# Optimization experiments

Measured on AMD Instinct MI355X. Metric: run time of the kernel, lower is better.

The kernel has to match this reference:

```python
import jax, jax.numpy as jnp
import numpy as np


def setup_inputs() -> dict:
    key = jax.random.key(0)
    k1, k2, k3, k4 = jax.random.split(key, 4)
    B, F, E = 8, 64, 50000
    Cout, K = 128, 5
    x = jax.random.normal(k1, (B, F, E), dtype=jnp.float32)
    gemm = jax.random.randint(k2, (B, E, 4), 0, E, dtype=jnp.int64)  # 1-ring neighbor edge indices
    fan_in = F * K
    W = jax.random.normal(k3, (Cout, F, 1, K), dtype=jnp.float32) / np.sqrt(fan_in)
    b = jax.random.normal(k4, (Cout,), dtype=jnp.float32) * 0.01
    return {"x": x, "gemm": gemm, "W": W, "b": b}


def reference(x, gemm, W, b):
    # x: [B, F, E] edge features; gemm: [B, E, 4] neighbor indices in [0, E)
    B, F, E = x.shape
    # pad_gemm prepends the edge's own index as column 0; create_gemm shifts by +1
    # and pads x with a zero column at index 0 (slot for missing / -1 neighbors).
    xp = jnp.concatenate([jnp.zeros((B, F, 1), dtype=x.dtype), x], axis=2)  # [B, F, E+1]
    self_idx = jnp.broadcast_to(jnp.arange(E, dtype=gemm.dtype)[None, :, None], (B, E, 1))
    idx = jnp.concatenate([self_idx, gemm], axis=2) + 1  # [B, E, 5], indices into E+1 slots
    # gather: f[b, f, e, k] = xp[b, f, idx[b, e, k]]
    xp_t = jnp.transpose(xp, (0, 2, 1))  # [B, E+1, F]
    f = jnp.take_along_axis(xp_t, idx.reshape(B, E * 5, 1), axis=1)  # [B, E*5, F]
    f = jnp.transpose(f.reshape(B, E, 5, F), (0, 3, 1, 2))  # [B, F, E, 5]
    # symmetric (order-invariant) pooling over the 4 neighbors
    x0 = f[:, :, :, 0]
    x1 = f[:, :, :, 1] + f[:, :, :, 3]
    x2 = f[:, :, :, 2] + f[:, :, :, 4]
    x3 = jnp.abs(f[:, :, :, 1] - f[:, :, :, 3])
    x4 = jnp.abs(f[:, :, :, 2] - f[:, :, :, 4])
    G = jnp.stack([x0, x1, x2, x3, x4], axis=3)  # [B, F, E, 5]
    # Conv2d with kernel (1, 5) over width-5 map == contraction over (F, 5)
    out = jnp.einsum('bfek,ofk->boe', G, W[:, :, 0, :]) + b[None, :, None]
    return out[..., None]  # [B, Cout, E, 1]
```

## Files before the change

kernel.cpp:

```cpp
#include <hip/hip_runtime.h>
#include <hip/hip_bf16.h>

#define NB 8
#define NF 64
#define NE 50000
#define NO 128
#define TE 64
#define NK 320
#define KSTEPS 10

typedef short short8 __attribute__((ext_vector_type(8)));
typedef float f32x4 __attribute__((ext_vector_type(4)));

__device__ __forceinline__ unsigned short f2bf(float x) {
    union { float f; unsigned int u; } v; v.f = x;
    unsigned int r = v.u + 0x7fffu + ((v.u >> 16) & 1u);
    return (unsigned short)(r >> 16);
}

__global__ __launch_bounds__(256) void transpose_x(
    const float* __restrict__ x, float* __restrict__ xT, int E)
{
    __shared__ float tile[64][65];
    int ntiles = (E + 63) >> 6;
    int b = blockIdx.x / ntiles;
    int t = blockIdx.x % ntiles;
    int e0 = t << 6;
    int le = threadIdx.x & 63;
    int q  = threadIdx.x >> 6;
    const float* xb = x + (size_t)b * NF * E;
    #pragma unroll
    for (int i = 0; i < 16; ++i) {
        int f = q * 16 + i;
        int e = e0 + le;
        tile[f][le] = (e < E) ? xb[(size_t)f * E + e] : 0.0f;
    }
    __syncthreads();
    float* xTb = xT + (size_t)b * E * NF;
    #pragma unroll
    for (int i = 0; i < 16; ++i) {
        int el = q * 16 + i;
        int e = e0 + el;
        if (e < E) xTb[(size_t)e * NF + le] = tile[le][el];
    }
}

__global__ __launch_bounds__(256) void prep_w(
    const float* __restrict__ W, unsigned short* __restrict__ Wt)
{
    int idx = blockIdx.x * 256 + threadIdx.x;
    if (idx >= NK * NO) return;
    int K = idx >> 7;
    int o = idx & 127;
    int f  = K & 63;
    int kp = K >> 6;
    float v = W[(size_t)o * (NF * 5) + f * 5 + kp];
    Wt[((size_t)(K >> 3) * NO + o) * 8 + (K & 7)] = f2bf(v);
}

__global__ __launch_bounds__(256) void conv_main(
    const float* __restrict__ xsrc,
    const int* __restrict__ gemm,
    const unsigned short* __restrict__ Wt,
    const float* __restrict__ bias,
    float* __restrict__ out,
    int E, int useXT)
{
    __shared__ __align__(16) unsigned short Gs[NK * TE];

    int ntiles = (E + TE - 1) / TE;
    int b     = blockIdx.x / ntiles;
    int etile = blockIdx.x % ntiles;
    int tid = threadIdx.x;

    {
        int ge = tid >> 2;
        int j  = tid & 3;
        int e  = etile * TE + ge;
        bool valid = (e < E);
        int gi[5];
        if (valid) {
            gi[0] = e;
            const int* gp = gemm + ((size_t)b * E + e) * 4;
            gi[1] = gp[0]; gi[2] = gp[1]; gi[3] = gp[2]; gi[4] = gp[3];
        }
        #pragma unroll
        for (int h = 0; h < 2; ++h) {
            int f0 = j * 16 + h * 8;
            float c[5][8];
            if (valid) {
                if (useXT) {
                    #pragma unroll
                    for (int k = 0; k < 5; ++k) {
                        const float* p = xsrc + ((size_t)b * E + gi[k]) * NF + f0;
                        float4 v0 = *(const float4*)p;
                        float4 v1 = *(const float4*)(p + 4);
                        c[k][0] = v0.x; c[k][1] = v0.y; c[k][2] = v0.z; c[k][3] = v0.w;
                        c[k][4] = v1.x; c[k][5] = v1.y; c[k][6] = v1.z; c[k][7] = v1.w;
                    }
                } else {
                    #pragma unroll
                    for (int k = 0; k < 5; ++k)
                        #pragma unroll
                        for (int i = 0; i < 8; ++i)
                            c[k][i] = xsrc[(size_t)b * NF * E + (size_t)(f0 + i) * E + gi[k]];
                }
            } else {
                #pragma unroll
                for (int k = 0; k < 5; ++k)
                    #pragma unroll
                    for (int i = 0; i < 8; ++i) c[k][i] = 0.0f;
            }
            float g[5][8];
            #pragma unroll
            for (int i = 0; i < 8; ++i) {
                g[0][i] = c[0][i];
                g[1][i] = c[1][i] + c[3][i];
                g[2][i] = c[2][i] + c[4][i];
                g[3][i] = fabsf(c[1][i] - c[3][i]);
                g[4][i] = fabsf(c[2][i] - c[4][i]);
            }
            #pragma unroll
            for (int kp = 0; kp < 5; ++kp) {
                int kblk = kp * 8 + j * 2 + h;
                uint4 pk;
                pk.x = (unsigned)f2bf(g[kp][0]) | ((unsigned)f2bf(g[kp][1]) << 16);
                pk.y = (unsigned)f2bf(g[kp][2]) | ((unsigned)f2bf(g[kp][3]) << 16);
                pk.z = (unsigned)f2bf(g[kp][4]) | ((unsigned)f2bf(g[kp][5]) << 16);
                pk.w = (unsigned)f2bf(g[kp][6]) | ((unsigned)f2bf(g[kp][7]) << 16);
                *(uint4*)&Gs[((size_t)kblk * TE + ge) * 8] = pk;
            }
        }
    }
    __syncthreads();

    int wave = tid >> 6;
    int lane = tid & 63;
    int l16 = lane & 15;
    int lq  = lane >> 4;
    int mh = (wave >> 1) * 4;
    int np = (wave & 1) * 2;

    f32x4 acc[4][2];
    #pragma unroll
    for (int mt = 0; mt < 4; ++mt)
        #pragma unroll
        for (int nt = 0; nt < 2; ++nt)
            acc[mt][nt] = (f32x4){0.f, 0.f, 0.f, 0.f};

    for (int ks = 0; ks < KSTEPS; ++ks) {
        short8 a[4], bb[2];
        #pragma unroll
        for (int mt = 0; mt < 4; ++mt) {
            int o = (mh + mt) * 16 + l16;
            a[mt] = *(const short8*)&Wt[((size_t)(ks * 4 + lq) * NO + o) * 8];
        }
        #pragma unroll
        for (int nt = 0; nt < 2; ++nt) {
            int el = (np + nt) * 16 + l16;
            bb[nt] = *(const short8*)&Gs[((size_t)(ks * 4 + lq) * TE + el) * 8];
        }
        #pragma unroll
        for (int mt = 0; mt < 4; ++mt)
            #pragma unroll
            for (int nt = 0; nt < 2; ++nt)
                acc[mt][nt] = __builtin_amdgcn_mfma_f32_16x16x32_bf16(
                    a[mt], bb[nt], acc[mt][nt], 0, 0, 0);
    }

    #pragma unroll
    for (int mt = 0; mt < 4; ++mt) {
        #pragma unroll
        for (int nt = 0; nt < 2; ++nt) {
            int el = (np + nt) * 16 + l16;
            int e  = etile * TE + el;
            if (e < E) {
                #pragma unroll
                for (int r = 0; r < 4; ++r) {
                    int o = (mh + mt) * 16 + lq * 4 + r;
                    out[((size_t)b * NO + o) * E + e] = acc[mt][nt][r] + bias[o];
                }
            }
        }
    }
}

extern "C" void kernel_launch(void* const* d_in, const int* in_sizes, int n_in,
                              void* d_out, int out_size, void* d_ws, size_t ws_size,
                              hipStream_t stream)
{
    const float* x    = (const float*)d_in[0];
    const int*   gemm = (const int*)d_in[1];
    const float* W    = (const float*)d_in[2];
    const float* bias = (const float*)d_in[3];
    float* out = (float*)d_out;

    const int E = NE;
    unsigned short* Wt = (unsigned short*)d_ws;
    size_t xT_off = 131072;
    float* xT = (float*)((char*)d_ws + xT_off);
    size_t need = xT_off + (size_t)NB * E * NF * sizeof(float);
    int useXT = (ws_size >= need) ? 1 : 0;

    prep_w<<<(NK * NO + 255) / 256, 256, 0, stream>>>(W, Wt);

    int ntiles = (E + TE - 1) / TE;
    if (useXT)
        transpose_x<<<NB * ntiles, 256, 0, stream>>>(x, xT, E);

    conv_main<<<NB * ntiles, 256, 0, stream>>>(
        useXT ? xT : x, gemm, Wt, bias, out, E, useXT);
}
```

Measured before the change: 418.4 us.

## Store transposed x in bf16 and feed gathered features straight into MFMA registers

The transpose kernel now writes x as bf16 instead of fp32, which halves the transposed buffer's write traffic and the bytes the gather reads back. The conv kernel drops the shared-memory G tile and its barrier. Each wave gathers its own 16 edges, builds the pooled features in registers as MFMA B operands, and loops over all 128 outputs while loading W fragments directly from global memory. Costs: the pooling arithmetic now runs on bf16-rounded inputs, adding extra rounding, and the ws-size fallback path is gone, so the kernel assumes the workspace is large enough.

```diff
diff --git a/kernel.cpp b/kernel.cpp
--- a/kernel.cpp
+++ b/kernel.cpp
@@ -5,9 +5,7 @@
 #define NF 64
 #define NE 50000
 #define NO 128
-#define TE 64
 #define NK 320
-#define KSTEPS 10
 
 typedef short short8 __attribute__((ext_vector_type(8)));
 typedef float f32x4 __attribute__((ext_vector_type(4)));
@@ -17,9 +15,12 @@
     unsigned int r = v.u + 0x7fffu + ((v.u >> 16) & 1u);
     return (unsigned short)(r >> 16);
 }
+__device__ __forceinline__ float bf2f(unsigned short h) {
+    union { unsigned int u; float f; } v; v.u = ((unsigned int)h) << 16; return v.f;
+}
 
 __global__ __launch_bounds__(256) void transpose_x(
-    const float* __restrict__ x, float* __restrict__ xT, int E)
+    const float* __restrict__ x, unsigned short* __restrict__ xT, int E)
 {
     __shared__ float tile[64][65];
     int ntiles = (E + 63) >> 6;
@@ -36,12 +37,18 @@
         tile[f][le] = (e < E) ? xb[(size_t)f * E + e] : 0.0f;
     }
     __syncthreads();
-    float* xTb = xT + (size_t)b * E * NF;
+    unsigned short* xTb = xT + (size_t)b * E * NF;
+    int fp = (threadIdx.x & 31) * 2;
+    int es = threadIdx.x >> 5;
     #pragma unroll
-    for (int i = 0; i < 16; ++i) {
-        int el = q * 16 + i;
+    for (int i = 0; i < 8; ++i) {
+        int el = i * 8 + es;
         int e = e0 + el;
-        if (e < E) xTb[(size_t)e * NF + le] = tile[le][el];
+        if (e < E) {
+            unsigned int pk = (unsigned int)f2bf(tile[fp][el])
+                            | ((unsigned int)f2bf(tile[fp + 1][el]) << 16);
+            *(unsigned int*)&xTb[(size_t)e * NF + fp] = pk;
+        }
     }
 }
 
@@ -59,127 +66,86 @@
 }
 
 __global__ __launch_bounds__(256) void conv_main(
-    const float* __restrict__ xsrc,
+    const unsigned short* __restrict__ xT,
     const int* __restrict__ gemm,
     const unsigned short* __restrict__ Wt,
     const float* __restrict__ bias,
     float* __restrict__ out,
-    int E, int useXT)
+    int E)
 {
-    __shared__ __align__(16) unsigned short Gs[NK * TE];
-
-    int ntiles = (E + TE - 1) / TE;
+    int ntiles = (E + 63) >> 6;
     int b     = blockIdx.x / ntiles;
     int etile = blockIdx.x % ntiles;
-    int tid = threadIdx.x;
+    int tid  = threadIdx.x;
+    int wave = tid >> 6;
+    int lane = tid & 63;
+    int l16  = lane & 15;
+    int lq   = lane >> 4;
 
-    {
-        int ge = tid >> 2;
-        int j  = tid & 3;
-        int e  = etile * TE + ge;
-        bool valid = (e < E);
-        int gi[5];
-        if (valid) {
-            gi[0] = e;
-            const int* gp = gemm + ((size_t)b * E + e) * 4;
-            gi[1] = gp[0]; gi[2] = gp[1]; gi[3] = gp[2]; gi[4] = gp[3];
+    int e = etile * 64 + wave * 16 + l16;
+    bool valid = (e < E);
+    int eC = valid ? e : (E - 1);
+
+    int gi[5];
+    gi[0] = eC;
+    int4 gv = *(const int4*)(gemm + ((size_t)b * E + eC) * 4);
+    gi[1] = gv.x; gi[2] = gv.y; gi[3] = gv.z; gi[4] = gv.w;
+
+    f32x4 acc[8];
+    #pragma unroll
+    for (int mt = 0; mt < 8; ++mt) acc[mt] = (f32x4){0.f, 0.f, 0.f, 0.f};
+
+    const unsigned short* xb = xT + (size_t)b * E * NF;
+
+    #pragma unroll
+    for (int half = 0; half < 2; ++half) {
+        int f0 = half * 32 + lq * 8;
+        uint4 craw[5];
+        #pragma unroll
+        for (int k = 0; k < 5; ++k)
+            craw[k] = *(const uint4*)&xb[(size_t)gi[k] * NF + f0];
+
+        const unsigned short* c1 = (const unsigned short*)&craw[1];
+        const unsigned short* c2 = (const unsigned short*)&craw[2];
+        const unsigned short* c3 = (const unsigned short*)&craw[3];
+        const unsigned short* c4 = (const unsigned short*)&craw[4];
+
+        short8 g[5];
+        g[0] = *(short8*)&craw[0];
+        unsigned short gb[4][8];
+        #pragma unroll
+        for (int i = 0; i < 8; ++i) {
+            float a1 = bf2f(c1[i]), a2 = bf2f(c2[i]);
+            float a3 = bf2f(c3[i]), a4 = bf2f(c4[i]);
+            gb[0][i] = f2bf(a1 + a3);
+            gb[1][i] = f2bf(a2 + a4);
+            gb[2][i] = f2bf(fabsf(a1 - a3));
+            gb[3][i] = f2bf(fabsf(a2 - a4));
         }
+        g[1] = *(short8*)&gb[0][0];
+        g[2] = *(short8*)&gb[1][0];
+        g[3] = *(short8*)&gb[2][0];
+        g[4] = *(short8*)&gb[3][0];
+
         #pragma unroll
-        for (int h = 0; h < 2; ++h) {
-            int f0 = j * 16 + h * 8;
-            float c[5][8];
-            if (valid) {
-                if (useXT) {
-                    #pragma unroll
-                    for (int k = 0; k < 5; ++k) {
-                        const float* p = xsrc + ((size_t)b * E + gi[k]) * NF + f0;
-                        float4 v0 = *(const float4*)p;
-                        float4 v1 = *(const float4*)(p + 4);
-                        c[k][0] = v0.x; c[k][1] = v0.y; c[k][2] = v0.z; c[k][3] = v0.w;
-                        c[k][4] = v1.x; c[k][5] = v1.y; c[k][6] = v1.z; c[k][7] = v1.w;
-                    }
-                } else {
-                    #pragma unroll
-                    for (int k = 0; k < 5; ++k)
-                        #pragma unroll
-                        for (int i = 0; i < 8; ++i)
-                            c[k][i] = xsrc[(size_t)b * NF * E + (size_t)(f0 + i) * E + gi[k]];
-                }
-            } else {
-                #pragma unroll
-                for (int k = 0; k < 5; ++k)
-                    #pragma unroll
-                    for (int i = 0; i < 8; ++i) c[k][i] = 0.0f;
-            }
-            float g[5][8];
+        for (int kp = 0; kp < 5; ++kp) {
+            int ks = kp * 2 + half;
+            const unsigned short* wp = Wt + (size_t)(ks * 4 + lq) * NO * 8;
             #pragma unroll
-            for (int i = 0; i < 8; ++i) {
-                g[0][i] = c[0][i];
-                g[1][i] = c[1][i] + c[3][i];
-                g[2][i] = c[2][i] + c[4][i];
-                g[3][i] = fabsf(c[1][i] - c[3][i]);
-                g[4][i] = fabsf(c[2][i] - c[4][i]);
-            }
-            #pragma unroll
-            for (int kp = 0; kp < 5; ++kp) {
-                int kblk = kp * 8 + j * 2 + h;
-                uint4 pk;
-                pk.x = (unsigned)f2bf(g[kp][0]) | ((unsigned)f2bf(g[kp][1]) << 16);
-                pk.y = (unsigned)f2bf(g[kp][2]) | ((unsigned)f2bf(g[kp][3]) << 16);
-                pk.z = (unsigned)f2bf(g[kp][4]) | ((unsigned)f2bf(g[kp][5]) << 16);
-                pk.w = (unsigned)f2bf(g[kp][6]) | ((unsigned)f2bf(g[kp][7]) << 16);
-                *(uint4*)&Gs[((size_t)kblk * TE + ge) * 8] = pk;
+            for (int mt = 0; mt < 8; ++mt) {
+                short8 a = *(const short8*)&wp[(mt * 16 + l16) * 8];
+                acc[mt] = __builtin_amdgcn_mfma_f32_16x16x32_bf16(a, g[kp], acc[mt], 0, 0, 0);
             }
         }
     }
-    __syncthreads();
 
-    int wave = tid >> 6;
-    int lane = tid & 63;
-    int l16 = lane & 15;
-    int lq  = lane >> 4;
-    int mh = (wave >> 1) * 4;
-    int np = (wave & 1) * 2;
-
-    f32x4 acc[4][2];
-    #pragma unroll
-    for (int mt = 0; mt < 4; ++mt)
+    if (valid) {
         #pragma unroll
-        for (int nt = 0; nt < 2; ++nt)
-            acc[mt][nt] = (f32x4){0.f, 0.f, 0.f, 0.f};
-
-    for (int ks = 0; ks < KSTEPS; ++ks) {
-        short8 a[4], bb[2];
-        #pragma unroll
-        for (int mt = 0; mt < 4; ++mt) {
-            int o = (mh + mt) * 16 + l16;
-            a[mt] = *(const short8*)&Wt[((size_t)(ks * 4 + lq) * NO + o) * 8];
-        }
-        #pragma unroll
-        for (int nt = 0; nt < 2; ++nt) {
-            int el = (np + nt) * 16 + l16;
-            bb[nt] = *(const short8*)&Gs[((size_t)(ks * 4 + lq) * TE + el) * 8];
-        }
-        #pragma unroll
-        for (int mt = 0; mt < 4; ++mt)
+        for (int mt = 0; mt < 8; ++mt) {
             #pragma unroll
-            for (int nt = 0; nt < 2; ++nt)
-                acc[mt][nt] = __builtin_amdgcn_mfma_f32_16x16x32_bf16(
-                    a[mt], bb[nt], acc[mt][nt], 0, 0, 0);
-    }
-
-    #pragma unroll
-    for (int mt = 0; mt < 4; ++mt) {
-        #pragma unroll
-        for (int nt = 0; nt < 2; ++nt) {
-            int el = (np + nt) * 16 + l16;
-            int e  = etile * TE + el;
-            if (e < E) {
-                #pragma unroll
-                for (int r = 0; r < 4; ++r) {
-                    int o = (mh + mt) * 16 + lq * 4 + r;
-                    out[((size_t)b * NO + o) * E + e] = acc[mt][nt][r] + bias[o];
-                }
+            for (int r = 0; r < 4; ++r) {
+                int o = mt * 16 + lq * 4 + r;
+                out[((size_t)b * NO + o) * E + e] = acc[mt][r] + bias[o];
             }
         }
     }
@@ -197,17 +163,12 @@
 
     const int E = NE;
     unsigned short* Wt = (unsigned short*)d_ws;
-    size_t xT_off = 131072;
-    float* xT = (float*)((char*)d_ws + xT_off);
-    size_t need = xT_off + (size_t)NB * E * NF * sizeof(float);
-    int useXT = (ws_size >= need) ? 1 : 0;
+    unsigned short* xT = (unsigned short*)((char*)d_ws + 131072);
 
     prep_w<<<(NK * NO + 255) / 256, 256, 0, stream>>>(W, Wt);
 
-    int ntiles = (E + TE - 1) / TE;
-    if (useXT)
-        transpose_x<<<NB * ntiles, 256, 0, stream>>>(x, xT, E);
+    int ntiles = (E + 63) / 64;
+    transpose_x<<<NB * ntiles, 256, 0, stream>>>(x, xT, E);
 
-    conv_main<<<NB * ntiles, 256, 0, stream>>>(
-        useXT ? xT : x, gemm, Wt, bias, out, E, useXT);
+    conv_main<<<NB * ntiles, 256, 0, stream>>>(xT, gemm, Wt, bias, out, E);
 }
```

After: 413.8 us. No clear change (-1.1%).
